# Kernel tuning notes

Measured on AMD Instinct MI355X. Metric: run time of the kernel, lower is better.

## Reference

```python
import jax, jax.numpy as jnp
import numpy as np


def setup_inputs() -> dict:
    key = jax.random.key(0)
    ks = jax.random.split(key, 6)
    T, B, E = 2048, 4, 768
    x = jax.random.normal(ks[0], (T, B, E), dtype=jnp.float32)
    key_padding_mask = jax.random.randint(ks[1], (T, B), 0, 2).astype(jnp.bool_)
    attn_bias = jax.random.normal(ks[2], (T, B), dtype=jnp.float32)  # (src_len, bsz)
    in_proj_weight = jax.random.normal(ks[3], (3 * E, E), dtype=jnp.float32) * 0.02
    in_proj_bias = jnp.zeros((3 * E,), dtype=jnp.float32)
    out_weight = jax.random.normal(ks[4], (E, E), dtype=jnp.float32) * 0.02
    out_bias = jnp.zeros((E,), dtype=jnp.float32)
    return {
        "x": x,
        "key_padding_mask": key_padding_mask,
        "attn_bias": attn_bias,
        "in_proj_weight": in_proj_weight,
        "in_proj_bias": in_proj_bias,
        "out_weight": out_weight,
        "out_bias": out_bias,
        "num_heads": 12,
    }


def reference(x, key_padding_mask, attn_bias, in_proj_weight, in_proj_bias,
              out_weight, out_bias, num_heads):
    T, B, E = x.shape
    H = num_heads
    Dh = E // H
    scaling = Dh ** (-0.5)

    # fused QKV projection (self-attention path: q=k=v=x)
    qkv = x @ in_proj_weight.T + in_proj_bias        # (T, B, 3E)
    q, k, v = jnp.split(qkv, 3, axis=-1)             # each (T, B, E)
    q = q * scaling

    # (T, B, E) -> (B, H, T, Dh)
    def to_heads(t):
        return t.reshape(T, B, H, Dh).transpose(1, 2, 0, 3)
    q, k, v = to_heads(q), to_heads(k), to_heads(v)

    # scores: (B, H, T_tgt, T_src)
    scores = jnp.einsum('bhtd,bhsd->bhts', q, k)
    scores = scores + attn_bias.T[:, None, None, :]              # bias over src
    neg_inf = jnp.asarray(-jnp.inf, dtype=scores.dtype)
    scores = jnp.where(key_padding_mask.T[:, None, None, :], neg_inf, scores)

    weights = jax.nn.softmax(scores, axis=-1)
    attn = jnp.einsum('bhts,bhsd->bhtd', weights, v)             # (B, H, T, Dh)
    attn = attn.transpose(2, 0, 1, 3).reshape(T, B, E)           # (T, B, E)
    out = attn @ out_weight.T + out_bias
    return out
```

## Files before the change

### kernel.cpp

```cpp
#include <hip/hip_runtime.h>
#include <math.h>

#define T_LEN 2048
#define BSZ   4
#define EMB   768
#define NH    12
#define DH    64
#define NTOK  (T_LEN * BSZ)
#define N_QKV (3 * EMB)
#define BH    (BSZ * NH)

typedef _Float16 f16;
typedef _Float16 f16x8 __attribute__((ext_vector_type(8)));
typedef float    f32x4 __attribute__((ext_vector_type(4)));

#define MFMA16(a, b, c) __builtin_amdgcn_mfma_f32_16x16x32_f16(a, b, c, 0, 0, 0)

__device__ __forceinline__ void gload16(const void* g, void* l) {
    __builtin_amdgcn_global_load_lds(
        (const __attribute__((address_space(1))) void*)g,
        (__attribute__((address_space(3))) void*)l, 16, 0, 0);
}

__global__ __launch_bounds__(256) void conv3(
    const float* __restrict__ s0, const float* __restrict__ s1,
    const float* __restrict__ s2, int n0, int n1, int n2,
    f16* __restrict__ dst)
{
    const int gid = blockIdx.x * 256 + threadIdx.x;
    const int i = gid * 4;
    const int t01 = n0 + n1;
    const float* s;
    int off;
    if (i < n0)            { s = s0; off = i; }
    else if (i < t01)      { s = s1; off = i - n0; }
    else if (i < t01 + n2) { s = s2; off = i - t01; }
    else return;
    const float4 v = *(const float4*)(s + off);
    f16 hv[4] = {(f16)v.x, (f16)v.y, (f16)v.z, (f16)v.w};
    *(double*)(dst + i) = *(double*)hv;
}

__global__ __launch_bounds__(64) void compact_mask(
    const int* __restrict__ mask, const float* __restrict__ abias,
    int* __restrict__ cidx, float* __restrict__ cbias,
    int* __restrict__ imap, int* __restrict__ ccount)
{
    const int b = blockIdx.x;
    const int lane = threadIdx.x;
    int* ip = cidx + b * T_LEN;
    float* bp = cbias + b * T_LEN;
    int* mp = imap + b * T_LEN;

    int base = 0;
    for (int c = 0; c < T_LEN / 64; ++c) {
        const int s = c * 64 + lane;
        const int mv = mask[s * BSZ + b];
        const float bv = abias[s * BSZ + b];
        const unsigned long long bal = __ballot(mv == 0);
        const int pos = __popcll(bal & ((1ull << lane) - 1ull));
        if (mv == 0) { ip[base + pos] = s; bp[base + pos] = bv; mp[s] = base + pos; }
        else mp[s] = -1;
        base += __popcll(bal);
    }
    const int npad = (base + 63) & ~63;
    if (lane < npad - base) { ip[base + lane] = 0; bp[base + lane] = -1e30f; }
    if (lane == 0) ccount[b] = npad;
}

template <int MODE>
__global__ __launch_bounds__(256) void gemm_h(
    const f16* __restrict__ A, const f16* __restrict__ W,
    const float* __restrict__ bias, float* __restrict__ C,
    f16* __restrict__ qb, f16* __restrict__ kc, f16* __restrict__ vb,
    const int* __restrict__ imap, int M, int N, int K)
{
    __shared__ __align__(16) f16 As[128][32];
    __shared__ __align__(16) f16 Bs[128][32];

    const int tid = threadIdx.x;
    const int w = tid >> 6, l = tid & 63;
    const int wr = w >> 1, wc = w & 1;
    const int lg = l >> 4, lr = l & 15;

    const int bm = blockIdx.x * 128, bn = blockIdx.y * 128;

    int srow[2], sqc[2];
#pragma unroll
    for (int it = 0; it < 2; ++it) {
        const int c = w * 128 + it * 64 + l;
        srow[it] = c >> 2;
        sqc[it] = (c & 3) ^ ((srow[it] >> 1) & 3);
    }

    f32x4 acc[4][4];
#pragma unroll
    for (int i = 0; i < 4; ++i)
#pragma unroll
        for (int j = 0; j < 4; ++j) acc[i][j] = (f32x4)(0.f);

    const int cq = lg ^ ((lr >> 1) & 3);

    for (int kt = 0; kt < K; kt += 32) {
        __syncthreads();
#pragma unroll
        for (int it = 0; it < 2; ++it) {
            const int ldsb = (w * 128 + it * 64) * 16;
            gload16(A + (size_t)(bm + srow[it]) * K + kt + sqc[it] * 8,
                    (char*)&As[0][0] + ldsb);
            gload16(W + (size_t)(bn + srow[it]) * K + kt + sqc[it] * 8,
                    (char*)&Bs[0][0] + ldsb);
        }
        __syncthreads();

        f16x8 af[4], bf[4];
#pragma unroll
        for (int am = 0; am < 4; ++am)
            af[am] = *(const f16x8*)((const char*)&As[0][0] +
                     (wr * 64 + am * 16 + lr) * 64 + cq * 16);
#pragma unroll
        for (int bnf = 0; bnf < 4; ++bnf)
            bf[bnf] = *(const f16x8*)((const char*)&Bs[0][0] +
                      (wc * 64 + bnf * 16 + lr) * 64 + cq * 16);
#pragma unroll
        for (int am = 0; am < 4; ++am)
#pragma unroll
            for (int bnf = 0; bnf < 4; ++bnf)
                acc[am][bnf] = MFMA16(af[am], bf[bnf], acc[am][bnf]);
    }

    const int colb = bn + wc * 64;
    const int rowb = bm + wr * 64;
    float bv[4];
#pragma unroll
    for (int j = 0; j < 4; ++j) bv[j] = bias[colb + j * 16 + lr];

    if (MODE == 0) {
#pragma unroll
        for (int am = 0; am < 4; ++am)
#pragma unroll
            for (int bnf = 0; bnf < 4; ++bnf)
#pragma unroll
                for (int rg = 0; rg < 4; ++rg) {
                    const int row = rowb + am * 16 + lg * 4 + rg;
                    const int col = colb + bnf * 16 + lr;
                    C[(size_t)row * N + col] = acc[am][bnf][rg] + bv[bnf];
                }
    } else {
        const int sec = bn / EMB;
        const float scale = (sec == 0) ? 0.125f : 1.0f;
#pragma unroll
        for (int bnf = 0; bnf < 4; ++bnf) {
            const int col = colb + bnf * 16 + lr;
            const int e = col - sec * EMB;
            const int h = e >> 6, d = e & 63;
#pragma unroll
            for (int am = 0; am < 4; ++am)
#pragma unroll
                for (int rg = 0; rg < 4; ++rg) {
                    const int row = rowb + am * 16 + lg * 4 + rg;
                    const int t = row >> 2, b = row & 3;
                    const f16 val = (f16)((acc[am][bnf][rg] + bv[bnf]) * scale);
                    if (sec == 0) {
                        qb[((size_t)((b * NH + h) * T_LEN + t)) * DH + d] = val;
                    } else if (sec == 1) {
                        const int ip = imap[b * T_LEN + t];
                        if (ip >= 0)
                            kc[((size_t)((b * NH + h) * T_LEN + ip)) * DH + d] = val;
                    } else {
                        vb[((size_t)((b * NH + h) * T_LEN + t)) * DH + d] = val;
                    }
                }
        }
    }
}

__global__ __launch_bounds__(256) void gather_vT(
    const f16* __restrict__ vb, const int* __restrict__ cidx,
    const int* __restrict__ ccnt, f16* __restrict__ vct)
{
    __shared__ f16 Vl[64][72];
    const int bh = blockIdx.y, b = bh / NH;
    const int i0 = blockIdx.x * 64;
    if (i0 >= ccnt[b]) return;
    const int tid = threadIdx.x;
    const size_t base = (size_t)bh * T_LEN * DH;

#pragma unroll
    for (int half = 0; half < 2; ++half) {
        const int c = half * 256 + tid;
        const int row = c >> 3, cc = c & 7;
        const int src = cidx[b * T_LEN + i0 + row];
        *(int4*)&Vl[row][cc * 8] =
            *(const int4*)(vb + base + (size_t)src * DH + cc * 8);
    }
    __syncthreads();
    const int dr = tid >> 2, ic = tid & 3;
    f16 tmp[16];
#pragma unroll
    for (int jj = 0; jj < 16; ++jj) tmp[jj] = Vl[ic * 16 + jj][dr];
    f16* dst = vct + ((size_t)bh * DH + dr) * T_LEN + i0 + ic * 16;
    *(int4*)(dst)     = *(int4*)&tmp[0];
    *(int4*)(dst + 8) = *(int4*)&tmp[8];
}

__global__ __launch_bounds__(256) void attn_mfma(
    const f16* __restrict__ qh, const f16* __restrict__ kcb,
    const f16* __restrict__ vct, const float* __restrict__ cbias,
    const int* __restrict__ ccnt, f16* __restrict__ abh)
{
    __shared__ __align__(16) f16 Kt[64][64];
    __shared__ __align__(16) f16 Vt[64][64];
    __shared__ __align__(16) f16 Pl[4][32][72];
    __shared__ float bias_l[64];

    const int bh = blockIdx.y, b = bh / NH, h = bh % NH;
    const int tid = threadIdx.x, w = tid >> 6, l = tid & 63;
    const int lg = l >> 4, lr = l & 15;
    const size_t base = (size_t)bh * T_LEN * DH;
    const int q0 = blockIdx.x * 128 + w * 32;

    f16x8 qf[2][2];
#pragma unroll
    for (int mi = 0; mi < 2; ++mi)
#pragma unroll
        for (int ki = 0; ki < 2; ++ki)
            qf[mi][ki] = *(const f16x8*)(qh + base +
                (size_t)(q0 + mi * 16 + lr) * DH + ki * 32 + lg * 8);

    f32x4 o[2][4];
#pragma unroll
    for (int mi = 0; mi < 2; ++mi)
#pragma unroll
        for (int bn = 0; bn < 4; ++bn) o[mi][bn] = (f32x4)(0.f);
    float mrow[2][4], lrow[2][4];
#pragma unroll
    for (int mi = 0; mi < 2; ++mi)
#pragma unroll
        for (int rg = 0; rg < 4; ++rg) { mrow[mi][rg] = -1e30f; lrow[mi][rg] = 0.f; }

    const int npad = ccnt[b];
    const float* biasp = cbias + b * T_LEN;
    const f16* kbase = kcb + base;
    const f16* vtbase = vct + (size_t)bh * DH * T_LEN;

    int srow[2], scc[2];
#pragma unroll
    for (int it = 0; it < 2; ++it) {
        const int c = w * 128 + it * 64 + l;
        srow[it] = c >> 3;
        scc[it] = (c & 7) ^ (srow[it] & 7);
    }

    for (int i0 = 0; i0 < npad; i0 += 64) {
        __syncthreads();
#pragma unroll
        for (int it = 0; it < 2; ++it) {
            const int ldsb = (w * 128 + it * 64) * 16;
            gload16(kbase + (size_t)(i0 + srow[it]) * DH + scc[it] * 8,
                    (char*)&Kt[0][0] + ldsb);
            gload16(vtbase + (size_t)srow[it] * T_LEN + i0 + scc[it] * 8,
                    (char*)&Vt[0][0] + ldsb);
        }
        if (tid < 64) bias_l[tid] = biasp[i0 + tid];
        __syncthreads();

        f32x4 s[2][4];
#pragma unroll
        for (int mi = 0; mi < 2; ++mi)
#pragma unroll
            for (int ni = 0; ni < 4; ++ni) s[mi][ni] = (f32x4)(0.f);
#pragma unroll
        for (int ni = 0; ni < 4; ++ni) {
            const int row = ni * 16 + lr;
#pragma unroll
            for (int ki = 0; ki < 2; ++ki) {
                const int cq = (ki * 4 + lg) ^ (row & 7);
                const f16x8 kf = *(const f16x8*)((const char*)&Kt[0][0] +
                                 row * 128 + cq * 16);
#pragma unroll
                for (int mi = 0; mi < 2; ++mi)
                    s[mi][ni] = MFMA16(qf[mi][ki], kf, s[mi][ni]);
            }
        }

        float bcol[4];
#pragma unroll
        for (int ni = 0; ni < 4; ++ni) bcol[ni] = bias_l[ni * 16 + lr];

        float r_[2][4], p[2][4][4];
#pragma unroll
        for (int mi = 0; mi < 2; ++mi)
#pragma unroll
            for (int rg = 0; rg < 4; ++rg) {
                float sv[4];
#pragma unroll
                for (int ni = 0; ni < 4; ++ni) sv[ni] = s[mi][ni][rg] + bcol[ni];
                float mx = fmaxf(fmaxf(sv[0], sv[1]), fmaxf(sv[2], sv[3]));
                mx = fmaxf(mx, __shfl_xor(mx, 1));
                mx = fmaxf(mx, __shfl_xor(mx, 2));
                mx = fmaxf(mx, __shfl_xor(mx, 4));
                mx = fmaxf(mx, __shfl_xor(mx, 8));
                const float newm = fmaxf(mrow[mi][rg], mx);
                r_[mi][rg] = __expf(mrow[mi][rg] - newm);
                mrow[mi][rg] = newm;
                float ps = 0.f;
#pragma unroll
                for (int ni = 0; ni < 4; ++ni) {
                    p[mi][ni][rg] = __expf(sv[ni] - newm);
                    ps += p[mi][ni][rg];
                }
                ps += __shfl_xor(ps, 1);
                ps += __shfl_xor(ps, 2);
                ps += __shfl_xor(ps, 4);
                ps += __shfl_xor(ps, 8);
                lrow[mi][rg] = lrow[mi][rg] * r_[mi][rg] + ps;
            }

#pragma unroll
        for (int mi = 0; mi < 2; ++mi)
#pragma unroll
            for (int ni = 0; ni < 4; ++ni)
#pragma unroll
                for (int rg = 0; rg < 4; ++rg)
                    Pl[w][mi * 16 + lg * 4 + rg][ni * 16 + lr] = (f16)p[mi][ni][rg];

#pragma unroll
        for (int mi = 0; mi < 2; ++mi)
#pragma unroll
            for (int bn = 0; bn < 4; ++bn)
#pragma unroll
                for (int rg = 0; rg < 4; ++rg) o[mi][bn][rg] *= r_[mi][rg];

        f16x8 pf[2][2];
#pragma unroll
        for (int mi = 0; mi < 2; ++mi)
#pragma unroll
            for (int ki = 0; ki < 2; ++ki)
                pf[mi][ki] = *(const f16x8*)((const char*)&Pl[w][0][0] +
                             (mi * 16 + lr) * 144 + ki * 64 + lg * 16);
#pragma unroll
        for (int bn = 0; bn < 4; ++bn) {
            const int row = bn * 16 + lr;
#pragma unroll
            for (int ki = 0; ki < 2; ++ki) {
                const int cq = (ki * 4 + lg) ^ (row & 7);
                const f16x8 vf = *(const f16x8*)((const char*)&Vt[0][0] +
                                 row * 128 + cq * 16);
#pragma unroll
                for (int mi = 0; mi < 2; ++mi)
                    o[mi][bn] = MFMA16(pf[mi][ki], vf, o[mi][bn]);
            }
        }
    }

#pragma unroll
    for (int mi = 0; mi < 2; ++mi)
#pragma unroll
        for (int rg = 0; rg < 4; ++rg) {
            const float inv = 1.f / lrow[mi][rg];
            const int q = q0 + mi * 16 + lg * 4 + rg;
#pragma unroll
            for (int bn = 0; bn < 4; ++bn) {
                const int col = h * DH + bn * 16 + lr;
                abh[(size_t)(q * BSZ + b) * EMB + col] = (f16)(o[mi][bn][rg] * inv);
            }
        }
}

extern "C" void kernel_launch(void* const* d_in, const int* in_sizes, int n_in,
                              void* d_out, int out_size, void* d_ws, size_t ws_size,
                              hipStream_t stream)
{
    const float* x     = (const float*)d_in[0];
    const int*   mask  = (const int*)d_in[1];
    const float* abias = (const float*)d_in[2];
    const float* wqkv  = (const float*)d_in[3];
    const float* bqkv  = (const float*)d_in[4];
    const float* wout  = (const float*)d_in[5];
    const float* bout  = (const float*)d_in[6];
    float* out = (float*)d_out;

    const int n_x  = NTOK * EMB;
    const int n_wq = N_QKV * EMB;
    const int n_wo = EMB * EMB;
    const size_t per = (size_t)BH * T_LEN * DH;

    f16* xh    = (f16*)d_ws;
    f16* wqkvh = xh + n_x;
    f16* wouth = wqkvh + n_wq;
    f16* qhb   = wouth + n_wo;
    f16* kcb   = qhb + per;
    f16* vhb   = kcb + per;
    f16* abh   = vhb + per;
    f16* vct   = abh + per;
    float* cbias = (float*)(vct + per);
    int*   cidx  = (int*)(cbias + BSZ * T_LEN);
    int*   imap  = cidx + BSZ * T_LEN;
    int*   ccnt  = imap + BSZ * T_LEN;

    compact_mask<<<BSZ, 64, 0, stream>>>(mask, abias, cidx, cbias, imap, ccnt);

    const int tot4 = (n_x + n_wq + n_wo) / 4;
    conv3<<<(tot4 + 255) / 256, 256, 0, stream>>>(
        x, wqkv, wout, n_x, n_wq, n_wo, xh);

    gemm_h<1><<<dim3(NTOK / 128, N_QKV / 128), 256, 0, stream>>>(
        xh, wqkvh, bqkv, nullptr, qhb, kcb, vhb, imap, NTOK, N_QKV, EMB);

    gather_vT<<<dim3(T_LEN / 64, BH), 256, 0, stream>>>(vhb, cidx, ccnt, vct);

    attn_mfma<<<dim3(T_LEN / 128, BH), 256, 0, stream>>>(
        qhb, kcb, vct, cbias, ccnt, abh);

    gemm_h<0><<<dim3(NTOK / 128, EMB / 128), 256, 0, stream>>>(
        abh, wouth, bout, out, nullptr, nullptr, nullptr, nullptr,
        NTOK, EMB, EMB);
}
```

Measured before the change: 302.3 us.

## Keep P in registers via transposed MFMA, double-buffer K/V, fuse mask compaction

The attention kernel now computes S transposed (K as the A operand), so each lane holds a column of probabilities that feed straight into a 16x16x16 MFMA for P·V. This removes the round trip of P through LDS and shortens the row reductions to two shuffles. K/V tiles and bias are double-buffered, so the next tile's global-to-LDS load overlaps compute with one barrier per iteration. Mask compaction is merged into the fp16 conversion launch, and its compaction uses a parallel 4-wave prefix. Together these save a launch and the serial scan, at the cost of more LDS per block and a smaller MFMA shape for P·V.

```diff
diff --git a/kernel.cpp b/kernel.cpp
--- a/kernel.cpp
+++ b/kernel.cpp
@@ -9,12 +9,15 @@
 #define NTOK  (T_LEN * BSZ)
 #define N_QKV (3 * EMB)
 #define BH    (BSZ * NH)
+#define CONVB 8448
 
 typedef _Float16 f16;
 typedef _Float16 f16x8 __attribute__((ext_vector_type(8)));
+typedef _Float16 f16x4 __attribute__((ext_vector_type(4)));
 typedef float    f32x4 __attribute__((ext_vector_type(4)));
 
-#define MFMA16(a, b, c) __builtin_amdgcn_mfma_f32_16x16x32_f16(a, b, c, 0, 0, 0)
+#define MFMA32(a, b, c) __builtin_amdgcn_mfma_f32_16x16x32_f16(a, b, c, 0, 0, 0)
+#define MFMA16(a, b, c) __builtin_amdgcn_mfma_f32_16x16x16f16(a, b, c, 0, 0, 0)
 
 __device__ __forceinline__ void gload16(const void* g, void* l) {
     __builtin_amdgcn_global_load_lds(
@@ -22,50 +25,66 @@
         (__attribute__((address_space(3))) void*)l, 16, 0, 0);
 }
 
-__global__ __launch_bounds__(256) void conv3(
+__global__ __launch_bounds__(256) void conv_compact(
     const float* __restrict__ s0, const float* __restrict__ s1,
-    const float* __restrict__ s2, int n0, int n1, int n2,
-    f16* __restrict__ dst)
-{
-    const int gid = blockIdx.x * 256 + threadIdx.x;
-    const int i = gid * 4;
-    const int t01 = n0 + n1;
-    const float* s;
-    int off;
-    if (i < n0)            { s = s0; off = i; }
-    else if (i < t01)      { s = s1; off = i - n0; }
-    else if (i < t01 + n2) { s = s2; off = i - t01; }
-    else return;
-    const float4 v = *(const float4*)(s + off);
-    f16 hv[4] = {(f16)v.x, (f16)v.y, (f16)v.z, (f16)v.w};
-    *(double*)(dst + i) = *(double*)hv;
-}
-
-__global__ __launch_bounds__(64) void compact_mask(
+    const float* __restrict__ s2, f16* __restrict__ dst,
     const int* __restrict__ mask, const float* __restrict__ abias,
     int* __restrict__ cidx, float* __restrict__ cbias,
     int* __restrict__ imap, int* __restrict__ ccount)
 {
-    const int b = blockIdx.x;
-    const int lane = threadIdx.x;
+    const int tid = threadIdx.x;
+    if (blockIdx.x < CONVB) {
+        const int n0 = NTOK * EMB, n1 = N_QKV * EMB, n2 = EMB * EMB;
+        const int i = (blockIdx.x * 256 + tid) * 4;
+        const int t01 = n0 + n1;
+        const float* s;
+        int off;
+        if (i < n0)            { s = s0; off = i; }
+        else if (i < t01)      { s = s1; off = i - n0; }
+        else if (i < t01 + n2) { s = s2; off = i - t01; }
+        else return;
+        const float4 v = *(const float4*)(s + off);
+        f16 hv[4] = {(f16)v.x, (f16)v.y, (f16)v.z, (f16)v.w};
+        *(double*)(dst + i) = *(double*)hv;
+        return;
+    }
+
+    const int b = blockIdx.x - CONVB;
+    __shared__ int cnt[32], off_l[32], tot[2];
+    const int wv = tid >> 6, lane = tid & 63;
     int* ip = cidx + b * T_LEN;
     float* bp = cbias + b * T_LEN;
     int* mp = imap + b * T_LEN;
 
-    int base = 0;
-    for (int c = 0; c < T_LEN / 64; ++c) {
+    for (int i = 0; i < 8; ++i) {
+        const int c = wv * 8 + i;
+        const int s = c * 64 + lane;
+        const int mv = mask[s * BSZ + b];
+        const unsigned long long bal = __ballot(mv == 0);
+        if (lane == 0) cnt[c] = __popcll(bal);
+    }
+    __syncthreads();
+    if (tid == 0) {
+        int acc = 0;
+        for (int c = 0; c < 32; ++c) { off_l[c] = acc; acc += cnt[c]; }
+        const int npad = (acc + 63) & ~63;
+        tot[0] = acc; tot[1] = npad;
+        ccount[b] = npad;
+    }
+    __syncthreads();
+    for (int i = 0; i < 8; ++i) {
+        const int c = wv * 8 + i;
         const int s = c * 64 + lane;
         const int mv = mask[s * BSZ + b];
         const float bv = abias[s * BSZ + b];
         const unsigned long long bal = __ballot(mv == 0);
         const int pos = __popcll(bal & ((1ull << lane) - 1ull));
-        if (mv == 0) { ip[base + pos] = s; bp[base + pos] = bv; mp[s] = base + pos; }
+        const int basec = off_l[c];
+        if (mv == 0) { ip[basec + pos] = s; bp[basec + pos] = bv; mp[s] = basec + pos; }
         else mp[s] = -1;
-        base += __popcll(bal);
-    }
-    const int npad = (base + 63) & ~63;
-    if (lane < npad - base) { ip[base + lane] = 0; bp[base + lane] = -1e30f; }
-    if (lane == 0) ccount[b] = npad;
+    }
+    const int baseT = tot[0], npad = tot[1];
+    if (tid < npad - baseT) { ip[baseT + tid] = 0; bp[baseT + tid] = -1e30f; }
 }
 
 template <int MODE>
@@ -126,7 +145,7 @@
         for (int am = 0; am < 4; ++am)
 #pragma unroll
             for (int bnf = 0; bnf < 4; ++bnf)
-                acc[am][bnf] = MFMA16(af[am], bf[bnf], acc[am][bnf]);
+                acc[am][bnf] = MFMA32(af[am], bf[bnf], acc[am][bnf]);
     }
 
     const int colb = bn + wc * 64;
@@ -159,16 +178,16 @@
 #pragma unroll
                 for (int rg = 0; rg < 4; ++rg) {
                     const int row = rowb + am * 16 + lg * 4 + rg;
-                    const int t = row >> 2, b = row & 3;
+                    const int t = row >> 2, bb = row & 3;
                     const f16 val = (f16)((acc[am][bnf][rg] + bv[bnf]) * scale);
                     if (sec == 0) {
-                        qb[((size_t)((b * NH + h) * T_LEN + t)) * DH + d] = val;
+                        qb[((size_t)((bb * NH + h) * T_LEN + t)) * DH + d] = val;
                     } else if (sec == 1) {
-                        const int ip = imap[b * T_LEN + t];
-                        if (ip >= 0)
-                            kc[((size_t)((b * NH + h) * T_LEN + ip)) * DH + d] = val;
+                        const int ipv = imap[bb * T_LEN + t];
+                        if (ipv >= 0)
+                            kc[((size_t)((bb * NH + h) * T_LEN + ipv)) * DH + d] = val;
                     } else {
-                        vb[((size_t)((b * NH + h) * T_LEN + t)) * DH + d] = val;
+                        vb[((size_t)((bb * NH + h) * T_LEN + t)) * DH + d] = val;
                     }
                 }
         }
@@ -209,10 +228,9 @@
     const f16* __restrict__ vct, const float* __restrict__ cbias,
     const int* __restrict__ ccnt, f16* __restrict__ abh)
 {
-    __shared__ __align__(16) f16 Kt[64][64];
-    __shared__ __align__(16) f16 Vt[64][64];
-    __shared__ __align__(16) f16 Pl[4][32][72];
-    __shared__ float bias_l[64];
+    __shared__ __align__(16) f16 Kt[2][64][64];
+    __shared__ __align__(16) f16 Vt[2][64][64];
+    __shared__ float bias_l[2][64];
 
     const int bh = blockIdx.y, b = bh / NH, h = bh % NH;
     const int tid = threadIdx.x, w = tid >> 6, l = tid & 63;
@@ -228,16 +246,12 @@
             qf[mi][ki] = *(const f16x8*)(qh + base +
                 (size_t)(q0 + mi * 16 + lr) * DH + ki * 32 + lg * 8);
 
-    f32x4 o[2][4];
-#pragma unroll
-    for (int mi = 0; mi < 2; ++mi)
-#pragma unroll
-        for (int bn = 0; bn < 4; ++bn) o[mi][bn] = (f32x4)(0.f);
-    float mrow[2][4], lrow[2][4];
-#pragma unroll
-    for (int mi = 0; mi < 2; ++mi)
-#pragma unroll
-        for (int rg = 0; rg < 4; ++rg) { mrow[mi][rg] = -1e30f; lrow[mi][rg] = 0.f; }
+    f32x4 o[4][2];
+#pragma unroll
+    for (int dt = 0; dt < 4; ++dt)
+#pragma unroll
+        for (int mi = 0; mi < 2; ++mi) o[dt][mi] = (f32x4)(0.f);
+    float m_[2] = {-1e30f, -1e30f}, l_[2] = {0.f, 0.f};
 
     const int npad = ccnt[b];
     const float* biasp = cbias + b * T_LEN;
@@ -252,120 +266,119 @@
         scc[it] = (c & 7) ^ (srow[it] & 7);
     }
 
-    for (int i0 = 0; i0 < npad; i0 += 64) {
-        __syncthreads();
+    auto stage = [&](int buf, int i0s) {
 #pragma unroll
         for (int it = 0; it < 2; ++it) {
             const int ldsb = (w * 128 + it * 64) * 16;
-            gload16(kbase + (size_t)(i0 + srow[it]) * DH + scc[it] * 8,
-                    (char*)&Kt[0][0] + ldsb);
-            gload16(vtbase + (size_t)srow[it] * T_LEN + i0 + scc[it] * 8,
-                    (char*)&Vt[0][0] + ldsb);
-        }
-        if (tid < 64) bias_l[tid] = biasp[i0 + tid];
-        __syncthreads();
-
-        f32x4 s[2][4];
-#pragma unroll
-        for (int mi = 0; mi < 2; ++mi)
-#pragma unroll
-            for (int ni = 0; ni < 4; ++ni) s[mi][ni] = (f32x4)(0.f);
+            gload16(kbase + (size_t)(i0s + srow[it]) * DH + scc[it] * 8,
+                    (char*)&Kt[buf][0][0] + ldsb);
+            gload16(vtbase + (size_t)srow[it] * T_LEN + i0s + scc[it] * 8,
+                    (char*)&Vt[buf][0][0] + ldsb);
+        }
+        if (tid < 64) bias_l[buf][tid] = biasp[i0s + tid];
+    };
+
+    stage(0, 0);
+    __syncthreads();
+
+    int cur = 0;
+    for (int i0 = 0; i0 < npad; i0 += 64, cur ^= 1) {
+        if (i0 + 64 < npad) stage(cur ^ 1, i0 + 64);
+
+        f32x4 s[4][2];
+#pragma unroll
+        for (int ni = 0; ni < 4; ++ni)
+#pragma unroll
+            for (int mi = 0; mi < 2; ++mi) s[ni][mi] = (f32x4)(0.f);
 #pragma unroll
         for (int ni = 0; ni < 4; ++ni) {
             const int row = ni * 16 + lr;
 #pragma unroll
             for (int ki = 0; ki < 2; ++ki) {
                 const int cq = (ki * 4 + lg) ^ (row & 7);
-                const f16x8 kf = *(const f16x8*)((const char*)&Kt[0][0] +
+                const f16x8 kf = *(const f16x8*)((const char*)&Kt[cur][0][0] +
                                  row * 128 + cq * 16);
 #pragma unroll
                 for (int mi = 0; mi < 2; ++mi)
-                    s[mi][ni] = MFMA16(qf[mi][ki], kf, s[mi][ni]);
+                    s[ni][mi] = MFMA32(kf, qf[mi][ki], s[ni][mi]);
             }
         }
 
-        float bcol[4];
-#pragma unroll
-        for (int ni = 0; ni < 4; ++ni) bcol[ni] = bias_l[ni * 16 + lr];
-
-        float r_[2][4], p[2][4][4];
-#pragma unroll
-        for (int mi = 0; mi < 2; ++mi)
-#pragma unroll
-            for (int rg = 0; rg < 4; ++rg) {
-                float sv[4];
-#pragma unroll
-                for (int ni = 0; ni < 4; ++ni) sv[ni] = s[mi][ni][rg] + bcol[ni];
-                float mx = fmaxf(fmaxf(sv[0], sv[1]), fmaxf(sv[2], sv[3]));
-                mx = fmaxf(mx, __shfl_xor(mx, 1));
-                mx = fmaxf(mx, __shfl_xor(mx, 2));
-                mx = fmaxf(mx, __shfl_xor(mx, 4));
-                mx = fmaxf(mx, __shfl_xor(mx, 8));
-                const float newm = fmaxf(mrow[mi][rg], mx);
-                r_[mi][rg] = __expf(mrow[mi][rg] - newm);
-                mrow[mi][rg] = newm;
-                float ps = 0.f;
-#pragma unroll
-                for (int ni = 0; ni < 4; ++ni) {
-                    p[mi][ni][rg] = __expf(sv[ni] - newm);
-                    ps += p[mi][ni][rg];
+        float bv[4][4];
+#pragma unroll
+        for (int ni = 0; ni < 4; ++ni) {
+            const float4 b4 = *(const float4*)&bias_l[cur][ni * 16 + lg * 4];
+            bv[ni][0] = b4.x; bv[ni][1] = b4.y; bv[ni][2] = b4.z; bv[ni][3] = b4.w;
+        }
+
+        f16x4 pk[2][4];
+        float r_[2];
+#pragma unroll
+        for (int mi = 0; mi < 2; ++mi) {
+            float sv[4][4];
+            float mx = -1e30f;
+#pragma unroll
+            for (int ni = 0; ni < 4; ++ni)
+#pragma unroll
+                for (int rg = 0; rg < 4; ++rg) {
+                    sv[ni][rg] = s[ni][mi][rg] + bv[ni][rg];
+                    mx = fmaxf(mx, sv[ni][rg]);
                 }
-                ps += __shfl_xor(ps, 1);
-                ps += __shfl_xor(ps, 2);
-                ps += __shfl_xor(ps, 4);
-                ps += __shfl_xor(ps, 8);
-                lrow[mi][rg] = lrow[mi][rg] * r_[mi][rg] + ps;
+            mx = fmaxf(mx, __shfl_xor(mx, 16));
+            mx = fmaxf(mx, __shfl_xor(mx, 32));
+            const float newm = fmaxf(m_[mi], mx);
+            r_[mi] = __expf(m_[mi] - newm);
+            m_[mi] = newm;
+            float ps = 0.f;
+#pragma unroll
+            for (int ni = 0; ni < 4; ++ni) {
+                float p0 = __expf(sv[ni][0] - newm);
+                float p1 = __expf(sv[ni][1] - newm);
+                float p2 = __expf(sv[ni][2] - newm);
+                float p3 = __expf(sv[ni][3] - newm);
+                ps += (p0 + p1) + (p2 + p3);
+                pk[mi][ni] = (f16x4){(f16)p0, (f16)p1, (f16)p2, (f16)p3};
             }
-
-#pragma unroll
-        for (int mi = 0; mi < 2; ++mi)
-#pragma unroll
-            for (int ni = 0; ni < 4; ++ni)
-#pragma unroll
-                for (int rg = 0; rg < 4; ++rg)
-                    Pl[w][mi * 16 + lg * 4 + rg][ni * 16 + lr] = (f16)p[mi][ni][rg];
-
-#pragma unroll
-        for (int mi = 0; mi < 2; ++mi)
-#pragma unroll
-            for (int bn = 0; bn < 4; ++bn)
-#pragma unroll
-                for (int rg = 0; rg < 4; ++rg) o[mi][bn][rg] *= r_[mi][rg];
-
-        f16x8 pf[2][2];
-#pragma unroll
-        for (int mi = 0; mi < 2; ++mi)
-#pragma unroll
-            for (int ki = 0; ki < 2; ++ki)
-                pf[mi][ki] = *(const f16x8*)((const char*)&Pl[w][0][0] +
-                             (mi * 16 + lr) * 144 + ki * 64 + lg * 16);
-#pragma unroll
-        for (int bn = 0; bn < 4; ++bn) {
-            const int row = bn * 16 + lr;
-#pragma unroll
-            for (int ki = 0; ki < 2; ++ki) {
-                const int cq = (ki * 4 + lg) ^ (row & 7);
-                const f16x8 vf = *(const f16x8*)((const char*)&Vt[0][0] +
-                                 row * 128 + cq * 16);
+            ps += __shfl_xor(ps, 16);
+            ps += __shfl_xor(ps, 32);
+            l_[mi] = l_[mi] * r_[mi] + ps;
+        }
+
+#pragma unroll
+        for (int dt = 0; dt < 4; ++dt)
+#pragma unroll
+            for (int mi = 0; mi < 2; ++mi)
+#pragma unroll
+                for (int rg = 0; rg < 4; ++rg) o[dt][mi][rg] *= r_[mi];
+
+#pragma unroll
+        for (int dt = 0; dt < 4; ++dt) {
+            const int row = dt * 16 + lr;
+#pragma unroll
+            for (int ni = 0; ni < 4; ++ni) {
+                const int swc = (ni * 2 + (lg >> 1)) ^ (row & 7);
+                const f16x4 vf = *(const f16x4*)((const char*)&Vt[cur][0][0] +
+                                 row * 128 + swc * 16 + (lg & 1) * 8);
 #pragma unroll
                 for (int mi = 0; mi < 2; ++mi)
-                    o[mi][bn] = MFMA16(pf[mi][ki], vf, o[mi][bn]);
+                    o[dt][mi] = MFMA16(vf, pk[mi][ni], o[dt][mi]);
             }
         }
-    }
-
-#pragma unroll
-    for (int mi = 0; mi < 2; ++mi)
-#pragma unroll
-        for (int rg = 0; rg < 4; ++rg) {
-            const float inv = 1.f / lrow[mi][rg];
-            const int q = q0 + mi * 16 + lg * 4 + rg;
-#pragma unroll
-            for (int bn = 0; bn < 4; ++bn) {
-                const int col = h * DH + bn * 16 + lr;
-                abh[(size_t)(q * BSZ + b) * EMB + col] = (f16)(o[mi][bn][rg] * inv);
-            }
-        }
+        __syncthreads();
+    }
+
+#pragma unroll
+    for (int mi = 0; mi < 2; ++mi) {
+        const float inv = 1.f / l_[mi];
+        const int q = q0 + mi * 16 + lr;
+#pragma unroll
+        for (int dt = 0; dt < 4; ++dt) {
+            const int d0 = dt * 16 + lg * 4;
+            f16x4 ov = {(f16)(o[dt][mi][0] * inv), (f16)(o[dt][mi][1] * inv),
+                        (f16)(o[dt][mi][2] * inv), (f16)(o[dt][mi][3] * inv)};
+            *(f16x4*)(abh + (size_t)(q * BSZ + b) * EMB + h * DH + d0) = ov;
+        }
+    }
 }
 
 extern "C" void kernel_launch(void* const* d_in, const int* in_sizes, int n_in,
@@ -399,11 +412,8 @@
     int*   imap  = cidx + BSZ * T_LEN;
     int*   ccnt  = imap + BSZ * T_LEN;
 
-    compact_mask<<<BSZ, 64, 0, stream>>>(mask, abias, cidx, cbias, imap, ccnt);
-
-    const int tot4 = (n_x + n_wq + n_wo) / 4;
-    conv3<<<(tot4 + 255) / 256, 256, 0, stream>>>(
-        x, wqkv, wout, n_x, n_wq, n_wo, xh);
+    conv_compact<<<CONVB + BSZ, 256, 0, stream>>>(
+        x, wqkv, wout, xh, mask, abias, cidx, cbias, imap, ccnt);
 
     gemm_h<1><<<dim3(NTOK / 128, N_QKV / 128), 256, 0, stream>>>(
         xh, wqkvh, bqkv, nullptr, qhb, kcb, vhb, imap, NTOK, N_QKV, EMB);
```

New measurement: 246.1 us. 18.6% less time.
